# Optimization experiments

Measured on AMD Instinct MI355X. Metric: run time of the kernel, lower is better.

The kernel has to match this reference:

```python
import jax, jax.numpy as jnp
import numpy as np

NEG_INF = -9e15  # same masking constant as the torch module


def setup_inputs() -> dict:
    key = jax.random.key(0)
    k1, k2, k3 = jax.random.split(key, 3)
    B, S, F = 8, 2048, 128
    H, D = 4, 32  # n_heads, head_dim = out_features // n_heads
    features = jax.random.normal(k1, (B, S, F), dtype=jnp.float32)
    adj_matrix = jax.random.randint(k2, (B, S, S), 0, 2, dtype=jnp.int32)
    # Xavier-uniform-ish init for W [H, F, D]
    limit = float(np.sqrt(6.0 / (F + D)))
    W = jax.random.uniform(k3, (H, F, D), dtype=jnp.float32, minval=-limit, maxval=limit)
    return {"features": features, "adj_matrix": adj_matrix, "W": W}


def reference(features, adj_matrix, W):
    # features: [B, S, F], adj_matrix: [B, S, S] (>0 == edge), W: [H, F, D]
    D = W.shape[-1]
    Wh = jnp.einsum("bsf,hfd->bhsd", features, W)                 # [B, H, S, D]
    scores = jnp.einsum("bhsd,bhtd->bhst", Wh, Wh) / jnp.sqrt(jnp.float32(D))
    scores = jnp.where(adj_matrix[:, None, :, :] > 0, scores, NEG_INF)
    attn = jax.nn.softmax(scores, axis=-1)                         # [B, H, S, S]
    # dropout is identity at inference (training=False)
    h = jnp.einsum("bhst,bhtd->bhsd", attn, Wh)                    # [B, H, S, D]
    B, H, S, _ = h.shape
    # concat heads along feature dim, matching torch.cat(heads, dim=2)
    return jnp.transpose(h, (0, 2, 1, 3)).reshape(B, S, H * D)
```

## Files before the change

kernel.cpp:

```cpp
#include <hip/hip_runtime.h>
#include <hip/hip_bf16.h>
#include <stdint.h>


namespace {
constexpr int S = 2048;
constexpr int F = 128;
constexpr int H = 4;
constexpr int D = 32;

typedef __attribute__((ext_vector_type(4))) float f32x4;
typedef __attribute__((ext_vector_type(8))) short s16x8;
typedef __attribute__((ext_vector_type(4))) short s16x4;

__device__ __forceinline__ short f2bf(float f) {
  __hip_bfloat16 h = __float2bfloat16(f);
  short s; __builtin_memcpy(&s, &h, sizeof(s)); return s;
}
__device__ __forceinline__ float bf2f(short s) {
  __hip_bfloat16 h; __builtin_memcpy(&h, &s, sizeof(s));
  return __bfloat162float(h);
}

__device__ __forceinline__ void gll16(const void* g, void* l) {
  __builtin_amdgcn_global_load_lds(
      (const __attribute__((address_space(1))) uint32_t*)(uintptr_t)g,
      (__attribute__((address_space(3))) uint32_t*)(uint32_t)(uintptr_t)l,
      16, 0, 0);
}

__global__ __launch_bounds__(256) void gat_proj(const float* __restrict__ feat,
                                                const float* __restrict__ W,
                                                short* __restrict__ Wh) {
  __shared__ __align__(16) short ftile[64][136];
  const int tid = threadIdx.x;
  const int w = tid >> 6;
  const int l = tid & 63;
  const int ln = l & 15, lg = l >> 4;
  const int row0 = blockIdx.x * 64;

#pragma unroll
  for (int i = 0; i < 4; ++i) {
    int c = i * 256 + tid;
    int r = c >> 4, c8 = (c & 15) * 8;
    const float* src = feat + (size_t)(row0 + r) * F + c8;
    float4 v0 = *(const float4*)src;
    float4 v1 = *(const float4*)(src + 4);
    s16x8 v;
    v[0]=f2bf(v0.x); v[1]=f2bf(v0.y); v[2]=f2bf(v0.z); v[3]=f2bf(v0.w);
    v[4]=f2bf(v1.x); v[5]=f2bf(v1.y); v[6]=f2bf(v1.z); v[7]=f2bf(v1.w);
    *(s16x8*)&ftile[r][c8] = v;
  }

  s16x8 bfr[4][2];
#pragma unroll
  for (int ks = 0; ks < 4; ++ks)
#pragma unroll
    for (int nt = 0; nt < 2; ++nt) {
      s16x8 v;
#pragma unroll
      for (int j = 0; j < 8; ++j)
        v[j] = f2bf(W[((size_t)w * F + ks*32 + lg*8 + j) * D + nt*16 + ln]);
      bfr[ks][nt] = v;
    }
  __syncthreads();

  const f32x4 z4 = {0.f, 0.f, 0.f, 0.f};
#pragma unroll
  for (int mt = 0; mt < 4; ++mt) {
    s16x8 a[4];
#pragma unroll
    for (int ks = 0; ks < 4; ++ks)
      a[ks] = *(const s16x8*)&ftile[mt*16 + ln][ks*32 + lg*8];
#pragma unroll
    for (int nt = 0; nt < 2; ++nt) {
      f32x4 c = z4;
#pragma unroll
      for (int ks = 0; ks < 4; ++ks)
        c = __builtin_amdgcn_mfma_f32_16x16x32_bf16(a[ks], bfr[ks][nt], c, 0, 0, 0);
#pragma unroll
      for (int r = 0; r < 4; ++r) {
        int srow = row0 + mt*16 + lg*4 + r;
        int b = srow >> 11, s = srow & (S - 1);
        Wh[(((size_t)b * H + w) * S + s) * D + nt*16 + ln] = f2bf(c[r]);
      }
    }
  }
}

__global__ __launch_bounds__(256, 2) void gat_attn(const int* __restrict__ adj,
                                                   const short* __restrict__ Wh,
                                                   float* __restrict__ out) {
  __shared__ __align__(16) int   adjm[2][32][64];
  __shared__ __align__(16) short vtt[H][2][32][64];
  __shared__ __align__(16) short ptl[H][32][64];

  const int tid = threadIdx.x;
  const int w = tid >> 6;
  const int l = tid & 63;
  const int ln = l & 15, lg = l >> 4, g4 = (l >> 4) * 4;
  const int e3 = ln & 7;
  const int b = blockIdx.x >> 6;
  const int s0 = (blockIdx.x & 63) * 32;

  const short* WhBH = Wh + ((size_t)b * H + w) * S * D;
  const int* adjB = adj + (size_t)b * S * S;
  short* pw = &ptl[w][0][0];

  const float cs = 0.25503486f;
  s16x8 qf[2];
#pragma unroll
  for (int qt = 0; qt < 2; ++qt) {
    s16x8 v = *(const s16x8*)&WhBH[(size_t)(s0 + qt*16 + ln) * D + lg*8];
    s16x8 o;
#pragma unroll
    for (int j = 0; j < 8; ++j) o[j] = f2bf(bf2f(v[j]) * cs);
    qf[qt] = o;
  }

  const f32x4 z4 = {0.f, 0.f, 0.f, 0.f};
  f32x4 accO[2][2];
#pragma unroll
  for (int i = 0; i < 2; ++i)
#pragma unroll
    for (int j = 0; j < 2; ++j) accO[i][j] = z4;
  float psum[2] = {0.f, 0.f};

#pragma unroll
  for (int i = 0; i < 2; ++i) {
    int r = w*8 + i*4 + (l >> 4);
    const int* src = adjB + (size_t)(s0 + r) * S + ((ln ^ (r & 7)) << 2);
    gll16(src, (char*)&adjm[0][0][0] + w*2048 + i*1024);
  }
  s16x8 kf[4];
#pragma unroll
  for (int mt = 0; mt < 4; ++mt)
    kf[mt] = *(const s16x8*)&WhBH[(size_t)(mt*16 + ln) * D + lg*8];
  {
    short* vb = &vtt[w][0][0][0];
#pragma unroll
    for (int mt = 0; mt < 4; ++mt) {
      int tg = mt*2 + (ln >> 3);
#pragma unroll
      for (int j = 0; j < 8; ++j) {
        int d = lg*8 + j;
        vb[d*64 + ((tg ^ ((j + lg) & 7)) << 3) + e3] = kf[mt][j];
      }
    }
  }
  __syncthreads();

  int cur = 0;
#pragma unroll 1
  for (int it = 0; it < S / 64; ++it) {
    const int nxt = cur ^ 1;
    const int t0n = (it + 1) * 64;
    const bool pf = (it < S / 64 - 1);

    if (pf) {
#pragma unroll
      for (int i = 0; i < 2; ++i) {
        int r = w*8 + i*4 + (l >> 4);
        const int* src = adjB + (size_t)(s0 + r) * S + t0n + ((ln ^ (r & 7)) << 2);
        gll16(src, (char*)&adjm[nxt][0][0] + w*2048 + i*1024);
      }
    }
    s16x8 kn[4];
    if (pf) {
#pragma unroll
      for (int mt = 0; mt < 4; ++mt)
        kn[mt] = *(const s16x8*)&WhBH[(size_t)(t0n + mt*16 + ln) * D + lg*8];
    }

    f32x4 accS[4][2];
#pragma unroll
    for (int mt = 0; mt < 4; ++mt)
#pragma unroll
      for (int qt = 0; qt < 2; ++qt)
        accS[mt][qt] = __builtin_amdgcn_mfma_f32_16x16x32_bf16(kf[mt], qf[qt], z4, 0, 0, 0);

#pragma unroll
    for (int mt = 0; mt < 4; ++mt) {
#pragma unroll
      for (int qt = 0; qt < 2; ++qt) {
        const int4 a = *(const int4*)&adjm[cur][qt*16 + ln][((mt*4 + lg) ^ e3) << 2];
        f32x4 sv = accS[mt][qt];
        float p0 = a.x ? __builtin_amdgcn_exp2f(sv[0]) : 0.f;
        float p1 = a.y ? __builtin_amdgcn_exp2f(sv[1]) : 0.f;
        float p2 = a.z ? __builtin_amdgcn_exp2f(sv[2]) : 0.f;
        float p3 = a.w ? __builtin_amdgcn_exp2f(sv[3]) : 0.f;
        psum[qt] += (p0 + p1) + (p2 + p3);
        s16x4 pk;
        pk[0] = f2bf(p0); pk[1] = f2bf(p1); pk[2] = f2bf(p2); pk[3] = f2bf(p3);
        int pg = mt*2 + (lg >> 1);
        *(s16x4*)&pw[(qt*16 + ln)*64 + ((pg ^ e3) << 3) + (lg & 1)*4] = pk;
      }
    }

    s16x8 ap[2][2];
#pragma unroll
    for (int qt = 0; qt < 2; ++qt)
#pragma unroll
      for (int kt = 0; kt < 2; ++kt)
        ap[qt][kt] = *(const s16x8*)&pw[(qt*16 + ln)*64 + (((kt*4 + lg) ^ e3) << 3)];

    const short* vr = &vtt[w][cur][0][0];
    s16x8 bv[2][2];
#pragma unroll
    for (int kt = 0; kt < 2; ++kt)
#pragma unroll
      for (int nt = 0; nt < 2; ++nt) {
        int dp = nt*16 + ln;
        int f = (ln + (ln >> 3) + 2*nt) & 7;
        bv[kt][nt] = *(const s16x8*)&vr[dp*64 + (((kt*4 + lg) ^ f) << 3)];
      }

#pragma unroll
    for (int qt = 0; qt < 2; ++qt)
#pragma unroll
      for (int nt = 0; nt < 2; ++nt)
#pragma unroll
        for (int kt = 0; kt < 2; ++kt)
          accO[qt][nt] = __builtin_amdgcn_mfma_f32_16x16x32_bf16(
              ap[qt][kt], bv[kt][nt], accO[qt][nt], 0, 0, 0);

    if (pf) {
      short* vb = &vtt[w][nxt][0][0];
#pragma unroll
      for (int mt = 0; mt < 4; ++mt) {
        int tg = mt*2 + (ln >> 3);
#pragma unroll
        for (int j = 0; j < 8; ++j) {
          int d = lg*8 + j;
          vb[d*64 + ((tg ^ ((j + lg) & 7)) << 3) + e3] = kn[mt][j];
        }
        kf[mt] = kn[mt];
      }
    }
    __syncthreads();
    cur = nxt;
  }

#pragma unroll
  for (int qt = 0; qt < 2; ++qt) {
    psum[qt] += __shfl_xor(psum[qt], 16, 64);
    psum[qt] += __shfl_xor(psum[qt], 32, 64);
  }
#pragma unroll
  for (int qt = 0; qt < 2; ++qt)
#pragma unroll
    for (int r = 0; r < 4; ++r) {
      float rs = __shfl(psum[qt], g4 + r, 16);
      float inv = 1.0f / rs;
#pragma unroll
      for (int nt = 0; nt < 2; ++nt)
        out[((size_t)b * S + s0 + qt*16 + g4 + r) * (H * D) + w*32 + nt*16 + ln]
            = accO[qt][nt][r] * inv;
    }
}

}

extern "C" void kernel_launch(void* const* d_in, const int* in_sizes, int n_in,
                              void* d_out, int out_size, void* d_ws, size_t ws_size,
                              hipStream_t stream) {
  const float* feat = (const float*)d_in[0];
  const int* adj    = (const int*)d_in[1];
  const float* W    = (const float*)d_in[2];
  float* out        = (float*)d_out;
  short* Wh         = (short*)d_ws;

  gat_proj<<<(8 * S) / 64, 256, 0, stream>>>(feat, W, Wh);
  gat_attn<<<8 * (S / 32), 256, 0, stream>>>(adj, Wh, out);
}
```

Before: 70.00 us.

## Emit transposed Wh from projection and load V fragments directly from global

The projection kernel now also writes a transposed copy of Wh (D×S per head). The attention kernel reads V operands for the PV MFMA straight from that copy into registers and swaps the MFMA operand order, so the per-iteration LDS transpose scatter of V goes away. The adjacency tile is loaded through registers and packed into bytes in a smaller LDS buffer instead of async global-to-LDS loads. Output stores become 16-byte vectors. In exchange there is an extra workspace write and more global reads per iteration, and the packing adds VGPR pressure.

Result: no change. 68.94 us (-1.5%).

```diff
diff --git a/kernel.cpp b/kernel.cpp
--- a/kernel.cpp
+++ b/kernel.cpp
@@ -22,22 +22,18 @@
   return __bfloat162float(h);
 }
 
-__device__ __forceinline__ void gll16(const void* g, void* l) {
-  __builtin_amdgcn_global_load_lds(
-      (const __attribute__((address_space(1))) uint32_t*)(uintptr_t)g,
-      (__attribute__((address_space(3))) uint32_t*)(uint32_t)(uintptr_t)l,
-      16, 0, 0);
-}
-
 __global__ __launch_bounds__(256) void gat_proj(const float* __restrict__ feat,
                                                 const float* __restrict__ W,
-                                                short* __restrict__ Wh) {
+                                                short* __restrict__ Wh,
+                                                short* __restrict__ WhT) {
   __shared__ __align__(16) short ftile[64][136];
   const int tid = threadIdx.x;
   const int w = tid >> 6;
   const int l = tid & 63;
-  const int ln = l & 15, lg = l >> 4;
+  const int ln = l & 15, lg = l >> 4, g4 = (l >> 4) * 4;
   const int row0 = blockIdx.x * 64;
+  const int b = row0 >> 11;
+  const int sl0 = row0 & (S - 1);
 
 #pragma unroll
   for (int i = 0; i < 4; ++i) {
@@ -78,21 +74,24 @@
 #pragma unroll
       for (int ks = 0; ks < 4; ++ks)
         c = __builtin_amdgcn_mfma_f32_16x16x32_bf16(a[ks], bfr[ks][nt], c, 0, 0, 0);
+      s16x4 tv;
 #pragma unroll
       for (int r = 0; r < 4; ++r) {
-        int srow = row0 + mt*16 + lg*4 + r;
-        int b = srow >> 11, s = srow & (S - 1);
-        Wh[(((size_t)b * H + w) * S + s) * D + nt*16 + ln] = f2bf(c[r]);
+        tv[r] = f2bf(c[r]);
+        int srow = row0 + mt*16 + g4 + r;
+        int s = srow & (S - 1);
+        Wh[(((size_t)b * H + w) * S + s) * D + nt*16 + ln] = tv[r];
       }
+      *(s16x4*)&WhT[(((size_t)b * H + w) * D + nt*16 + ln) * S + sl0 + mt*16 + g4] = tv;
     }
   }
 }
 
 __global__ __launch_bounds__(256, 2) void gat_attn(const int* __restrict__ adj,
                                                    const short* __restrict__ Wh,
+                                                   const short* __restrict__ WhT,
                                                    float* __restrict__ out) {
-  __shared__ __align__(16) int   adjm[2][32][64];
-  __shared__ __align__(16) short vtt[H][2][32][64];
+  __shared__ unsigned adjw[2][32][20];
   __shared__ __align__(16) short ptl[H][32][64];
 
   const int tid = threadIdx.x;
@@ -104,8 +103,14 @@
   const int s0 = (blockIdx.x & 63) * 32;
 
   const short* WhBH = Wh + ((size_t)b * H + w) * S * D;
+  const short* WhTBH = WhT + ((size_t)b * H + w) * D * S;
   const int* adjB = adj + (size_t)b * S * S;
   short* pw = &ptl[w][0][0];
+
+  const int ra = tid >> 4;
+  const int cg = tid & 15;
+  const int* adjR0 = adjB + (size_t)(s0 + ra) * S + cg * 4;
+  const int* adjR1 = adjB + (size_t)(s0 + 16 + ra) * S + cg * 4;
 
   const float cs = 0.25503486f;
   s16x8 qf[2];
@@ -126,50 +131,43 @@
     for (int j = 0; j < 2; ++j) accO[i][j] = z4;
   float psum[2] = {0.f, 0.f};
 
-#pragma unroll
-  for (int i = 0; i < 2; ++i) {
-    int r = w*8 + i*4 + (l >> 4);
-    const int* src = adjB + (size_t)(s0 + r) * S + ((ln ^ (r & 7)) << 2);
-    gll16(src, (char*)&adjm[0][0][0] + w*2048 + i*1024);
-  }
+  int4 a0 = *(const int4*)adjR0;
+  int4 a1 = *(const int4*)adjR1;
   s16x8 kf[4];
 #pragma unroll
   for (int mt = 0; mt < 4; ++mt)
     kf[mt] = *(const s16x8*)&WhBH[(size_t)(mt*16 + ln) * D + lg*8];
-  {
-    short* vb = &vtt[w][0][0][0];
-#pragma unroll
-    for (int mt = 0; mt < 4; ++mt) {
-      int tg = mt*2 + (ln >> 3);
-#pragma unroll
-      for (int j = 0; j < 8; ++j) {
-        int d = lg*8 + j;
-        vb[d*64 + ((tg ^ ((j + lg) & 7)) << 3) + e3] = kf[mt][j];
-      }
-    }
-  }
+  s16x8 av[2][2];
+#pragma unroll
+  for (int dt = 0; dt < 2; ++dt)
+#pragma unroll
+    for (int kt = 0; kt < 2; ++kt)
+      av[dt][kt] = *(const s16x8*)&WhTBH[(size_t)(dt*16 + ln) * S + kt*32 + lg*8];
+  adjw[0][ra][cg]      = (unsigned)a0.x | ((unsigned)a0.y << 8) |
+                         ((unsigned)a0.z << 16) | ((unsigned)a0.w << 24);
+  adjw[0][16 + ra][cg] = (unsigned)a1.x | ((unsigned)a1.y << 8) |
+                         ((unsigned)a1.z << 16) | ((unsigned)a1.w << 24);
   __syncthreads();
 
-  int cur = 0;
 #pragma unroll 1
   for (int it = 0; it < S / 64; ++it) {
-    const int nxt = cur ^ 1;
+    const int cur = it & 1, nxt = cur ^ 1;
     const int t0n = (it + 1) * 64;
     const bool pf = (it < S / 64 - 1);
 
+    int4 a0n, a1n;
+    s16x8 kn[4], avn[2][2];
     if (pf) {
-#pragma unroll
-      for (int i = 0; i < 2; ++i) {
-        int r = w*8 + i*4 + (l >> 4);
-        const int* src = adjB + (size_t)(s0 + r) * S + t0n + ((ln ^ (r & 7)) << 2);
-        gll16(src, (char*)&adjm[nxt][0][0] + w*2048 + i*1024);
-      }
-    }
-    s16x8 kn[4];
-    if (pf) {
+      a0n = *(const int4*)(adjR0 + t0n);
+      a1n = *(const int4*)(adjR1 + t0n);
 #pragma unroll
       for (int mt = 0; mt < 4; ++mt)
         kn[mt] = *(const s16x8*)&WhBH[(size_t)(t0n + mt*16 + ln) * D + lg*8];
+#pragma unroll
+      for (int dt = 0; dt < 2; ++dt)
+#pragma unroll
+        for (int kt = 0; kt < 2; ++kt)
+          avn[dt][kt] = *(const s16x8*)&WhTBH[(size_t)(dt*16 + ln) * S + t0n + kt*32 + lg*8];
     }
 
     f32x4 accS[4][2];
@@ -180,15 +178,16 @@
         accS[mt][qt] = __builtin_amdgcn_mfma_f32_16x16x32_bf16(kf[mt], qf[qt], z4, 0, 0, 0);
 
 #pragma unroll
-    for (int mt = 0; mt < 4; ++mt) {
-#pragma unroll
-      for (int qt = 0; qt < 2; ++qt) {
-        const int4 a = *(const int4*)&adjm[cur][qt*16 + ln][((mt*4 + lg) ^ e3) << 2];
+    for (int qt = 0; qt < 2; ++qt) {
+      const unsigned* ab = &adjw[cur][qt*16 + ln][lg];
+#pragma unroll
+      for (int mt = 0; mt < 4; ++mt) {
+        unsigned m = ab[mt*4];
         f32x4 sv = accS[mt][qt];
-        float p0 = a.x ? __builtin_amdgcn_exp2f(sv[0]) : 0.f;
-        float p1 = a.y ? __builtin_amdgcn_exp2f(sv[1]) : 0.f;
-        float p2 = a.z ? __builtin_amdgcn_exp2f(sv[2]) : 0.f;
-        float p3 = a.w ? __builtin_amdgcn_exp2f(sv[3]) : 0.f;
+        float p0 = (m & 0xffu)       ? __builtin_amdgcn_exp2f(sv[0]) : 0.f;
+        float p1 = (m & 0xff00u)     ? __builtin_amdgcn_exp2f(sv[1]) : 0.f;
+        float p2 = (m & 0xff0000u)   ? __builtin_amdgcn_exp2f(sv[2]) : 0.f;
+        float p3 = (m & 0xff000000u) ? __builtin_amdgcn_exp2f(sv[3]) : 0.f;
         psum[qt] += (p0 + p1) + (p2 + p3);
         s16x4 pk;
         pk[0] = f2bf(p0); pk[1] = f2bf(p1); pk[2] = f2bf(p2); pk[3] = f2bf(p3);
@@ -204,41 +203,28 @@
       for (int kt = 0; kt < 2; ++kt)
         ap[qt][kt] = *(const s16x8*)&pw[(qt*16 + ln)*64 + (((kt*4 + lg) ^ e3) << 3)];
 
-    const short* vr = &vtt[w][cur][0][0];
-    s16x8 bv[2][2];
-#pragma unroll
-    for (int kt = 0; kt < 2; ++kt)
-#pragma unroll
-      for (int nt = 0; nt < 2; ++nt) {
-        int dp = nt*16 + ln;
-        int f = (ln + (ln >> 3) + 2*nt) & 7;
-        bv[kt][nt] = *(const s16x8*)&vr[dp*64 + (((kt*4 + lg) ^ f) << 3)];
-      }
-
-#pragma unroll
-    for (int qt = 0; qt < 2; ++qt)
-#pragma unroll
-      for (int nt = 0; nt < 2; ++nt)
+#pragma unroll
+    for (int dt = 0; dt < 2; ++dt)
+#pragma unroll
+      for (int qt = 0; qt < 2; ++qt)
 #pragma unroll
         for (int kt = 0; kt < 2; ++kt)
-          accO[qt][nt] = __builtin_amdgcn_mfma_f32_16x16x32_bf16(
-              ap[qt][kt], bv[kt][nt], accO[qt][nt], 0, 0, 0);
+          accO[dt][qt] = __builtin_amdgcn_mfma_f32_16x16x32_bf16(
+              av[dt][kt], ap[qt][kt], accO[dt][qt], 0, 0, 0);
 
     if (pf) {
-      short* vb = &vtt[w][nxt][0][0];
-#pragma unroll
-      for (int mt = 0; mt < 4; ++mt) {
-        int tg = mt*2 + (ln >> 3);
-#pragma unroll
-        for (int j = 0; j < 8; ++j) {
-          int d = lg*8 + j;
-          vb[d*64 + ((tg ^ ((j + lg) & 7)) << 3) + e3] = kn[mt][j];
-        }
-        kf[mt] = kn[mt];
-      }
+      adjw[nxt][ra][cg]      = (unsigned)a0n.x | ((unsigned)a0n.y << 8) |
+                               ((unsigned)a0n.z << 16) | ((unsigned)a0n.w << 24);
+      adjw[nxt][16 + ra][cg] = (unsigned)a1n.x | ((unsigned)a1n.y << 8) |
+                               ((unsigned)a1n.z << 16) | ((unsigned)a1n.w << 24);
+#pragma unroll
+      for (int mt = 0; mt < 4; ++mt) kf[mt] = kn[mt];
+#pragma unroll
+      for (int dt = 0; dt < 2; ++dt)
+#pragma unroll
+        for (int kt = 0; kt < 2; ++kt) av[dt][kt] = avn[dt][kt];
     }
     __syncthreads();
-    cur = nxt;
   }
 
 #pragma unroll
@@ -247,16 +233,16 @@
     psum[qt] += __shfl_xor(psum[qt], 32, 64);
   }
 #pragma unroll
-  for (int qt = 0; qt < 2; ++qt)
-#pragma unroll
-    for (int r = 0; r < 4; ++r) {
-      float rs = __shfl(psum[qt], g4 + r, 16);
-      float inv = 1.0f / rs;
-#pragma unroll
-      for (int nt = 0; nt < 2; ++nt)
-        out[((size_t)b * S + s0 + qt*16 + g4 + r) * (H * D) + w*32 + nt*16 + ln]
-            = accO[qt][nt][r] * inv;
-    }
+  for (int qt = 0; qt < 2; ++qt) {
+    float inv = 1.0f / psum[qt];
+#pragma unroll
+    for (int dt = 0; dt < 2; ++dt) {
+      f32x4 o;
+#pragma unroll
+      for (int r = 0; r < 4; ++r) o[r] = accO[dt][qt][r] * inv;
+      *(f32x4*)&out[((size_t)b * S + s0 + qt*16 + ln) * (H * D) + w*32 + dt*16 + g4] = o;
+    }
+  }
 }
 
 }
@@ -269,7 +255,8 @@
   const float* W    = (const float*)d_in[2];
   float* out        = (float*)d_out;
   short* Wh         = (short*)d_ws;
-
-  gat_proj<<<(8 * S) / 64, 256, 0, stream>>>(feat, W, Wh);
-  gat_attn<<<8 * (S / 32), 256, 0, stream>>>(adj, Wh, out);
-}
+  short* WhT        = (short*)d_ws + (size_t)8 * H * S * D;
+
+  gat_proj<<<(8 * S) / 64, 256, 0, stream>>>(feat, W, Wh, WhT);
+  gat_attn<<<8 * (S / 32), 256, 0, stream>>>(adj, Wh, WhT, out);
+}
```
